# Kernel tuning notes

Measured on AMD Instinct MI355X. Metric: run time of the kernel, lower is better.

Reference implementation:

```python
import jax, jax.numpy as jnp
import numpy as np

MARGIN = 0.5
BETA = 0.0
K = 5

def setup_inputs() -> dict:
    key = jax.random.key(0)
    k1, k2 = jax.random.split(key)
    n, d, n_classes = 4096, 512, 512
    inputs = jax.random.normal(k1, (n, d), dtype=jnp.float32)
    # L2-normalize as is standard for similarity-based DML embeddings
    inputs = inputs / jnp.linalg.norm(inputs, axis=1, keepdims=True)
    targets = jax.random.randint(k2, (n,), 0, n_classes, dtype=jnp.int64)
    return {"inputs": inputs, "targets": targets}

def reference(inputs, targets):
    n = inputs.shape[0]
    sim = inputs @ inputs.T                      # [n, n] similarity matrix
    same = targets[:, None] == targets[None, :]  # [n, n] same-class mask
    eye = jnp.eye(n, dtype=bool)
    pos_mask = same & ~eye                       # positive pairs (off-diagonal)
    neg_mask = ~same                             # negative pairs
    # margin_loss (hinge on similarity): pos -> [margin + beta - s]_+, neg -> [margin + s - beta]_+
    pos_l = jnp.maximum(MARGIN + BETA - sim, 0.0)
    neg_l = jnp.maximum(MARGIN + sim - BETA, 0.0)
    valid = pos_mask | neg_mask
    pair_loss = jnp.where(pos_mask, pos_l, neg_l)  # per-pair loss where valid
    num_of_zeros = jnp.sum(valid & (pair_loss == 0.0))
    # top-(4K) over the multiset of all valid pair losses (== topk of concat(pos_loss, neg_loss))
    masked = jnp.where(valid, pair_loss, -jnp.inf).reshape(-1)
    top_loss, _ = jax.lax.top_k(masked, 4 * K)
    loss = jnp.mean(top_loss)
    mean_pos_sim = jnp.sum(jnp.where(pos_mask, sim, 0.0)) / jnp.sum(pos_mask)
    mean_neg_sim = jnp.sum(jnp.where(neg_mask, sim, 0.0)) / jnp.sum(neg_mask)
    # NOTE: the original swaps the names: it returns mean(pos_sim) as `mean_neg_sim` and vice versa.
    return (loss, num_of_zeros, mean_pos_sim, mean_neg_sim)
```

## Files before the change

kernel.cpp:

```cpp
#include <hip/hip_runtime.h>
#include <hip/hip_fp16.h>

constexpr int N = 4096;
constexpr int D = 512;
constexpr int NT = 64;
constexpr int NBLK = NT * (NT + 1) / 2;
constexpr int NSEG = 32;
constexpr int SEGSZ = NBLK / NSEG;
constexpr float SENT = -1e30f;
constexpr float CAND_TH = 0.64f;

typedef _Float16 f16x8 __attribute__((ext_vector_type(8)));
typedef float f32x4 __attribute__((ext_vector_type(4)));

#define WAITV16() asm volatile("s_waitcnt vmcnt(16)" ::: "memory")
#define WAITV0() asm volatile("s_waitcnt vmcnt(0)" ::: "memory")

__device__ __forceinline__ void load_lds16(const _Float16* g, _Float16* l) {
  __builtin_amdgcn_global_load_lds(
      (const __attribute__((address_space(1))) void*)g,
      (__attribute__((address_space(3))) void*)l, 16, 0, 0);
}

__device__ __forceinline__ void ins10(float (&t)[10], float v) {
#pragma unroll
  for (int k = 9; k > 0; k--) t[k] = fmaxf(t[k], fminf(v, t[k - 1]));
  t[0] = fmaxf(t[0], v);
}

template <int M>
__device__ __forceinline__ void wave_sel10(float (&vals)[M], float (&out)[10]) {
  int lane = threadIdx.x & 63;
  float lm = vals[0];
#pragma unroll
  for (int k = 1; k < M; k++) lm = fmaxf(lm, vals[k]);
#pragma unroll
  for (int r = 0; r < 10; r++) out[r] = SENT;
#pragma unroll
  for (int r = 0; r < 10; r++) {
    float wmx = lm;
#pragma unroll
    for (int ofs = 1; ofs < 64; ofs <<= 1)
      wmx = fmaxf(wmx, __shfl_xor(wmx, ofs));
    if (wmx == SENT) break;
    out[r] = wmx;
    unsigned long long b = __ballot(lm == wmx);
    int leader = __ffsll(b) - 1;
    if (lane == leader) {
      bool found = false;
#pragma unroll
      for (int k = 0; k < M; k++) {
        bool hit = !found && (vals[k] == wmx);
        vals[k] = hit ? SENT : vals[k];
        found = found || hit;
      }
      lm = vals[0];
#pragma unroll
      for (int k = 1; k < M; k++) lm = fmaxf(lm, vals[k]);
    }
  }
}

constexpr int TOP10G_OFF = 41600;
constexpr int STATSL2_OFF = 124800;
constexpr int T10L2_OFF = 125440;
constexpr int DONE2_OFF = 126720;
constexpr int XH_OFF = 126976;

__global__ void prep_kernel(const float4* __restrict__ X4,
                            ushort4* __restrict__ Xh4,
                            unsigned* __restrict__ done2) {
  int gid = blockIdx.x * 256 + threadIdx.x;
  if (gid == 0) *done2 = 0u;
  float4 v = X4[gid];
  ushort4 o;
  o.x = __half_as_ushort(__float2half_rn(v.x));
  o.y = __half_as_ushort(__float2half_rn(v.y));
  o.z = __half_as_ushort(__float2half_rn(v.z));
  o.w = __half_as_ushort(__float2half_rn(v.w));
  Xh4[gid] = o;
}

__global__ __launch_bounds__(64) void gemm_stats_kernel(
    const _Float16* __restrict__ Xh, const int* __restrict__ tgt,
    float* __restrict__ slots, float* __restrict__ top10g) {
  float* blk_sumv = slots;
  float* blk_sump = slots + NBLK;
  unsigned* blk_cntv = (unsigned*)(slots + 2 * NBLK);
  unsigned* blk_cntp = (unsigned*)(slots + 3 * NBLK);
  unsigned* blk_zero = (unsigned*)(slots + 4 * NBLK);

  __shared__ _Float16 As[2][64 * 64];
  __shared__ _Float16 Bs[2][64 * 64];

  int lane = threadIdx.x;

  int id = blockIdx.x, br = 0;
  while (id >= (NT - br)) { id -= (NT - br); br++; }
  int bc = br + id;

  int lrow = lane & 15;
  int q4 = lane >> 4;
  int quad4 = q4 * 4;
  int x7 = lrow & 7;

  int ti2[4][4], tj2[4];
#pragma unroll
  for (int ni = 0; ni < 4; ni++) tj2[ni] = tgt[bc * 64 + ni * 16 + lrow];
#pragma unroll
  for (int mi = 0; mi < 4; mi++)
#pragma unroll
    for (int r = 0; r < 4; r++) ti2[mi][r] = tgt[br * 64 + mi * 16 + quad4 + r];

  int rsub = lane >> 3;
  int gch = (lane & 7) ^ rsub;
  int goff[8];
#pragma unroll
  for (int i = 0; i < 8; i++)
    goff[i] = (i * 8 + rsub) * (D * 2) + gch * 16;
  const char* Ab = (const char*)(Xh + (size_t)(br * 64) * D);
  const char* Bb = (const char*)(Xh + (size_t)(bc * 64) * D);

  auto issue = [&](int k0b, int sel) {
#pragma unroll
    for (int i = 0; i < 8; i++) {
      load_lds16((const _Float16*)(Ab + goff[i] + k0b), &As[sel][i * 512]);
      load_lds16((const _Float16*)(Bb + goff[i] + k0b), &Bs[sel][i * 512]);
    }
  };

  f32x4 acc[4][4] = {};

  issue(0, 0);

  for (int it = 0; it < 8; ++it) {
    int sel = it & 1;
    if (it < 7) {
      issue((it + 1) * 128, sel ^ 1);
      WAITV16();
    } else {
      WAITV0();
    }
#pragma unroll
    for (int s = 0; s < 2; s++) {
      int pos = ((s * 4 + q4) ^ x7) * 8;
      f16x8 af[4], bf[4];
#pragma unroll
      for (int mi = 0; mi < 4; mi++)
        af[mi] = *(const f16x8*)&As[sel][(mi * 16 + lrow) * 64 + pos];
#pragma unroll
      for (int ni = 0; ni < 4; ni++)
        bf[ni] = *(const f16x8*)&Bs[sel][(ni * 16 + lrow) * 64 + pos];
#pragma unroll
      for (int mi = 0; mi < 4; mi++)
#pragma unroll
        for (int ni = 0; ni < 4; ni++)
          acc[mi][ni] = __builtin_amdgcn_mfma_f32_16x16x32_f16(
              af[mi], bf[ni], acc[mi][ni], 0, 0, 0);
    }
  }

  float lsv = 0.f, lsp = 0.f;
  unsigned lcv = 0, lcp = 0, lz = 0;
  int ib = br * 64 + quad4;
  int jb = bc * 64 + lrow;

  float t10[10];
#pragma unroll
  for (int k = 0; k < 10; k++) t10[k] = SENT;

#pragma unroll
  for (int mi = 0; mi < 4; mi++)
#pragma unroll
    for (int ni = 0; ni < 4; ni++)
#pragma unroll
      for (int r = 0; r < 4; r++) {
        float s = acc[mi][ni][r];
        int i = ib + mi * 16 + r;
        int j = jb + ni * 16;
        bool valid = j > i;
        bool pos = valid && (ti2[mi][r] == tj2[ni]);
        float t = pos ? -s : s;
        float loss = fmaxf(0.5f + t, 0.0f);
        if (valid) { lsv += s; lcv++; if (loss == 0.0f) lz++; }
        if (pos) { lsp += s; lcp++; }
        if (valid && (loss > CAND_TH)) ins10(t10, loss);
      }

#pragma unroll
  for (int o = 32; o > 0; o >>= 1) {
    lsv += __shfl_down(lsv, o);
    lsp += __shfl_down(lsp, o);
    lcv += __shfl_down(lcv, o);
    lcp += __shfl_down(lcp, o);
    lz  += __shfl_down(lz, o);
  }
  float w10[10];
  wave_sel10<10>(t10, w10);

  if (lane == 0) {
    int b = blockIdx.x;
    blk_sumv[b] = lsv;
    blk_sump[b] = lsp;
    blk_cntv[b] = lcv;
    blk_cntp[b] = lcp;
    blk_zero[b] = lz;
#pragma unroll
    for (int k = 0; k < 10; k++) top10g[b * 10 + k] = w10[k];
  }
}

__global__ __launch_bounds__(256) void finalize_kernel(
    const float* __restrict__ slots, const float* __restrict__ top10g,
    float* __restrict__ statsL2, float* __restrict__ t10L2,
    unsigned* __restrict__ done2, float* __restrict__ out) {
  const float* blk_sumv = slots;
  const float* blk_sump = slots + NBLK;
  const unsigned* blk_cntv = (const unsigned*)(slots + 2 * NBLK);
  const unsigned* blk_cntp = (const unsigned*)(slots + 3 * NBLK);
  const unsigned* blk_zero = (const unsigned*)(slots + 4 * NBLK);

  __shared__ float wml[40];
  __shared__ float redf[2][4];
  __shared__ unsigned redu[3][4];
  __shared__ int lastFlag;

  int tid = threadIdx.x;
  int lane = tid & 63, wave = tid >> 6;
  int f = blockIdx.x;

  float sv = 0.f, sp = 0.f;
  unsigned cv = 0, cp = 0, zz = 0;
  if (tid < SEGSZ) {
    int row = f * SEGSZ + tid;
    sv = blk_sumv[row]; sp = blk_sump[row];
    cv = blk_cntv[row]; cp = blk_cntp[row]; zz = blk_zero[row];
  }
#pragma unroll
  for (int o = 32; o > 0; o >>= 1) {
    sv += __shfl_down(sv, o);
    sp += __shfl_down(sp, o);
    cv += __shfl_down(cv, o);
    cp += __shfl_down(cp, o);
    zz += __shfl_down(zz, o);
  }
  if (lane == 0) {
    redf[0][wave] = sv; redf[1][wave] = sp;
    redu[0][wave] = cv; redu[1][wave] = cp; redu[2][wave] = zz;
  }

  float v3[3];
#pragma unroll
  for (int k = 0; k < 3; k++) {
    int g = tid + k * 256;
    v3[k] = (g < SEGSZ * 10) ? top10g[f * SEGSZ * 10 + g] : SENT;
  }
  float wl[10];
  wave_sel10<3>(v3, wl);
  if (lane == 0) {
#pragma unroll
    for (int r = 0; r < 10; r++) wml[wave * 10 + r] = wl[r];
  }
  __syncthreads();
  if (wave == 0) {
    float mv[1];
    mv[0] = (lane < 40) ? wml[lane] : SENT;
    float s10[10];
    wave_sel10<1>(mv, s10);
    if (lane == 0) {
      statsL2[f] = redf[0][0] + redf[0][1] + redf[0][2] + redf[0][3];
      statsL2[NSEG + f] = redf[1][0] + redf[1][1] + redf[1][2] + redf[1][3];
      ((unsigned*)statsL2)[2 * NSEG + f] =
          redu[0][0] + redu[0][1] + redu[0][2] + redu[0][3];
      ((unsigned*)statsL2)[3 * NSEG + f] =
          redu[1][0] + redu[1][1] + redu[1][2] + redu[1][3];
      ((unsigned*)statsL2)[4 * NSEG + f] =
          redu[2][0] + redu[2][1] + redu[2][2] + redu[2][3];
#pragma unroll
      for (int r = 0; r < 10; r++) t10L2[f * 10 + r] = s10[r];
    }
  }
  __syncthreads();

  if (tid == 0) {
    __threadfence();
    unsigned old = atomicAdd(done2, 1u);
    lastFlag = (old == NSEG - 1);
  }
  __syncthreads();
  if (!lastFlag) return;
  __threadfence();

  float sv2 = 0.f, sp2 = 0.f;
  unsigned cv2 = 0, cp2 = 0, zz2 = 0;
  if (tid < NSEG) {
    sv2 = statsL2[tid]; sp2 = statsL2[NSEG + tid];
    cv2 = ((const unsigned*)statsL2)[2 * NSEG + tid];
    cp2 = ((const unsigned*)statsL2)[3 * NSEG + tid];
    zz2 = ((const unsigned*)statsL2)[4 * NSEG + tid];
  }
#pragma unroll
  for (int o = 32; o > 0; o >>= 1) {
    sv2 += __shfl_down(sv2, o);
    sp2 += __shfl_down(sp2, o);
    cv2 += __shfl_down(cv2, o);
    cp2 += __shfl_down(cp2, o);
    zz2 += __shfl_down(zz2, o);
  }
  if (lane == 0) {
    redf[0][wave] = sv2; redf[1][wave] = sp2;
    redu[0][wave] = cv2; redu[1][wave] = cp2; redu[2][wave] = zz2;
  }

  float v2[2];
  v2[0] = (tid < NSEG * 10) ? t10L2[tid] : SENT;
  int g2 = tid + 256;
  v2[1] = (g2 < NSEG * 10) ? t10L2[g2] : SENT;
  float wl2[10];
  wave_sel10<2>(v2, wl2);
  if (lane == 0) {
#pragma unroll
    for (int r = 0; r < 10; r++) wml[wave * 10 + r] = wl2[r];
  }
  __syncthreads();

  if (wave == 0) {
    float mv[1];
    mv[0] = (lane < 40) ? wml[lane] : SENT;
    float f10[10];
    wave_sel10<1>(mv, f10);
    if (lane == 0) {
      float topsum = 0.f;
#pragma unroll
      for (int r = 0; r < 10; r++) topsum += f10[r];
      float tsv = redf[0][0] + redf[0][1] + redf[0][2] + redf[0][3];
      float tsp = redf[1][0] + redf[1][1] + redf[1][2] + redf[1][3];
      unsigned tcv = redu[0][0] + redu[0][1] + redu[0][2] + redu[0][3];
      unsigned tcp = redu[1][0] + redu[1][1] + redu[1][2] + redu[1][3];
      unsigned tzz = redu[2][0] + redu[2][1] + redu[2][2] + redu[2][3];
      out[0] = topsum * 0.1f;
      out[1] = (float)(2u * tzz);
      out[2] = tsp / (float)tcp;
      out[3] = (tsv - tsp) / (float)(tcv - tcp);
    }
  }
}

extern "C" void kernel_launch(void* const* d_in, const int* in_sizes, int n_in,
                              void* d_out, int out_size, void* d_ws, size_t ws_size,
                              hipStream_t stream) {
  const float* X = (const float*)d_in[0];
  const int* tgt = (const int*)d_in[1];
  float* out = (float*)d_out;
  char* ws = (char*)d_ws;

  float* slots = (float*)ws;
  float* top10g = (float*)(ws + TOP10G_OFF);
  float* statsL2 = (float*)(ws + STATSL2_OFF);
  float* t10L2 = (float*)(ws + T10L2_OFF);
  unsigned* done2 = (unsigned*)(ws + DONE2_OFF);
  _Float16* Xh = (_Float16*)(ws + XH_OFF);

  prep_kernel<<<(N * D / 4) / 256, 256, 0, stream>>>((const float4*)X,
                                                     (ushort4*)Xh, done2);
  gemm_stats_kernel<<<NBLK, 64, 0, stream>>>(Xh, tgt, slots, top10g);
  finalize_kernel<<<NSEG, 256, 0, stream>>>(slots, top10g, statsL2, t10L2,
                                            done2, out);
}
```

Measured before the change: 116.8 us.

## Load MFMA fragments directly from global memory, bypassing LDS staging

Removes the LDS double-buffered tiles filled by global_load_lds and instead has each lane load its f16x8 MFMA fragments straight from global memory into registers, with a register double buffer one k-step ahead. The goal is to drop the LDS round trip, the swizzle arithmetic and the explicit vmcnt waits, and to free LDS for occupancy. In exchange, global loads become 16-byte strided reads per lane, and latency hiding rests on one step of register prefetch and the L2/L1 caches.

```diff
diff --git a/kernel.cpp b/kernel.cpp
--- a/kernel.cpp
+++ b/kernel.cpp
@@ -12,15 +12,6 @@
 
 typedef _Float16 f16x8 __attribute__((ext_vector_type(8)));
 typedef float f32x4 __attribute__((ext_vector_type(4)));
-
-#define WAITV16() asm volatile("s_waitcnt vmcnt(16)" ::: "memory")
-#define WAITV0() asm volatile("s_waitcnt vmcnt(0)" ::: "memory")
-
-__device__ __forceinline__ void load_lds16(const _Float16* g, _Float16* l) {
-  __builtin_amdgcn_global_load_lds(
-      (const __attribute__((address_space(1))) void*)g,
-      (__attribute__((address_space(3))) void*)l, 16, 0, 0);
-}
 
 __device__ __forceinline__ void ins10(float (&t)[10], float v) {
 #pragma unroll
@@ -90,9 +81,6 @@
   unsigned* blk_cntp = (unsigned*)(slots + 3 * NBLK);
   unsigned* blk_zero = (unsigned*)(slots + 4 * NBLK);
 
-  __shared__ _Float16 As[2][64 * 64];
-  __shared__ _Float16 Bs[2][64 * 64];
-
   int lane = threadIdx.x;
 
   int id = blockIdx.x, br = 0;
@@ -102,7 +90,6 @@
   int lrow = lane & 15;
   int q4 = lane >> 4;
   int quad4 = q4 * 4;
-  int x7 = lrow & 7;
 
   int ti2[4][4], tj2[4];
 #pragma unroll
@@ -112,52 +99,32 @@
 #pragma unroll
     for (int r = 0; r < 4; r++) ti2[mi][r] = tgt[br * 64 + mi * 16 + quad4 + r];
 
-  int rsub = lane >> 3;
-  int gch = (lane & 7) ^ rsub;
-  int goff[8];
-#pragma unroll
-  for (int i = 0; i < 8; i++)
-    goff[i] = (i * 8 + rsub) * (D * 2) + gch * 16;
-  const char* Ab = (const char*)(Xh + (size_t)(br * 64) * D);
-  const char* Bb = (const char*)(Xh + (size_t)(bc * 64) * D);
-
-  auto issue = [&](int k0b, int sel) {
-#pragma unroll
-    for (int i = 0; i < 8; i++) {
-      load_lds16((const _Float16*)(Ab + goff[i] + k0b), &As[sel][i * 512]);
-      load_lds16((const _Float16*)(Bb + goff[i] + k0b), &Bs[sel][i * 512]);
-    }
+  const _Float16* Afrag = Xh + (size_t)(br * 64 + lrow) * D + q4 * 8;
+  const _Float16* Bfrag = Xh + (size_t)(bc * 64 + lrow) * D + q4 * 8;
+
+  f32x4 acc[4][4] = {};
+  f16x8 af[2][4], bf[2][4];
+
+  auto ldfrag = [&](int ks, int p) {
+#pragma unroll
+    for (int mi = 0; mi < 4; mi++)
+      af[p][mi] = *(const f16x8*)(Afrag + (size_t)(mi * 16) * D + ks);
+#pragma unroll
+    for (int ni = 0; ni < 4; ni++)
+      bf[p][ni] = *(const f16x8*)(Bfrag + (size_t)(ni * 16) * D + ks);
   };
 
-  f32x4 acc[4][4] = {};
-
-  issue(0, 0);
-
-  for (int it = 0; it < 8; ++it) {
-    int sel = it & 1;
-    if (it < 7) {
-      issue((it + 1) * 128, sel ^ 1);
-      WAITV16();
-    } else {
-      WAITV0();
-    }
-#pragma unroll
-    for (int s = 0; s < 2; s++) {
-      int pos = ((s * 4 + q4) ^ x7) * 8;
-      f16x8 af[4], bf[4];
-#pragma unroll
-      for (int mi = 0; mi < 4; mi++)
-        af[mi] = *(const f16x8*)&As[sel][(mi * 16 + lrow) * 64 + pos];
+  ldfrag(0, 0);
+#pragma unroll
+  for (int s = 0; s < 16; s++) {
+    int p = s & 1;
+    if (s < 15) ldfrag((s + 1) * 32, p ^ 1);
+#pragma unroll
+    for (int mi = 0; mi < 4; mi++)
 #pragma unroll
       for (int ni = 0; ni < 4; ni++)
-        bf[ni] = *(const f16x8*)&Bs[sel][(ni * 16 + lrow) * 64 + pos];
-#pragma unroll
-      for (int mi = 0; mi < 4; mi++)
-#pragma unroll
-        for (int ni = 0; ni < 4; ni++)
-          acc[mi][ni] = __builtin_amdgcn_mfma_f32_16x16x32_f16(
-              af[mi], bf[ni], acc[mi][ni], 0, 0, 0);
-    }
+        acc[mi][ni] = __builtin_amdgcn_mfma_f32_16x16x32_f16(
+            af[p][mi], bf[p][ni], acc[mi][ni], 0, 0, 0);
   }
 
   float lsv = 0.f, lsp = 0.f;
```

Result: slower. 134.0 us (+14.7%).
